# Kernel optimization log

Measured on AMD Instinct MI355X. Metric: run time of the kernel, lower is better.

Reference implementation:

```python
import math
import jax, jax.numpy as jnp
import numpy as np

B, S, M, D, H = 4, 1024, 8, 64, 8
NF = D // 2  # n_freq = head_dim // 2
BANDWIDTH = 1.0


def setup_inputs() -> dict:
    key = jax.random.key(0)
    ks = jax.random.split(key, 12)
    n = lambda k, shp, sc=1.0: (jax.random.normal(k, shp, dtype=jnp.float32) * sc)
    w_scale = 0.02  # typical init scale for linear weights
    return {
        'q_atoms': n(ks[0], (B, S, M, D)),
        'q_logw': n(ks[1], (B, S, M)),
        'k_atoms': n(ks[2], (B, S, M, D)),
        'k_logw': n(ks[3], (B, S, M)),
        'v_atoms': n(ks[4], (B, S, M, D)),
        'v_logw': n(ks[5], (B, S, M)),
        'Wq': n(ks[6], (H * D, D), w_scale),   # torch Linear weight [out, in]
        'Wk': n(ks[7], (H * D, D), w_scale),
        'Wv': n(ks[8], (H * D, D), w_scale),
        'Wo': n(ks[9], (D, H * D), w_scale),
        'Ww': n(ks[10], (M, D), w_scale * 0.1),  # w_proj.weight scaled by 0.1
        'freqs': n(ks[11], (H, D, NF), 1.0 / BANDWIDTH),  # buffer
    }


def reference(q_atoms, q_logw, k_atoms, k_logw, v_atoms, v_logw,
              Wq, Wk, Wv, Wo, Ww, freqs):
    rff_scale = 1.0 / math.sqrt(NF)
    attn_scale = 1.0 / math.sqrt(D)

    q_w = jax.nn.softmax(q_logw, axis=-1)  # [B,S,M]
    k_w = jax.nn.softmax(k_logw, axis=-1)

    def proj(x, W):  # x: [B,S,M,D], W: [H*D, D] -> [B,S,M,H,D]
        return jnp.einsum('bsmd,ed->bsme', x, W).reshape(B, -1, M, H, D)

    qa = proj(q_atoms, Wq)
    ka = proj(k_atoms, Wk)
    va = proj(v_atoms, Wv)  # [B,S,M,H,D]

    def rff_encode(atoms, weights):
        # atoms: [B,S,M,H,D], weights: [B,S,M] -> [B,H,S,F] with F=D
        p = jnp.einsum('bsmhd,hdf->bsmhf', atoms, freqs)
        phi = jnp.concatenate([jnp.cos(p), jnp.sin(p)], axis=-1) * rff_scale
        z = jnp.einsum('bsmhf,bsm->bshf', phi, weights)
        return z.transpose(0, 2, 1, 3)

    q_enc = rff_encode(qa, q_w)  # [B,H,S,D]
    k_enc = rff_encode(ka, k_w)

    attn = jax.nn.softmax(
        jnp.einsum('bhqf,bhkf->bhqk', q_enc, k_enc) * attn_scale, axis=-1)

    # attn @ values, keeping atom dim m: [B,S,M,H,D]
    out = jnp.einsum('bhqk,bkmhd->bqmhd', attn, va)
    out = out.reshape(B, S, M, H * D)
    out_atoms = out @ Wo.T                  # [B,S,M,D]
    out_features = out_atoms.mean(axis=2)   # [B,S,D]
    new_log_weights = q_logw + out_features @ Ww.T  # [B,S,M]
    return out_atoms, new_log_weights
```

## Files before the change

kernel.cpp:

```cpp
#include <hip/hip_runtime.h>
#include <hip/hip_bf16.h>

typedef __hip_bfloat16 bf16;
typedef __attribute__((ext_vector_type(8))) short short8;
typedef __attribute__((ext_vector_type(4))) float floatx4;

#define CB 4
#define CS 1024
#define CM 8
#define CD 64
#define CH 8
#define CNF 32
#define CHD 512

#define OB_STRIDE 520
#define OS_STRIDE 68
#define AT_STRIDE 72
#define VO_STRIDE 40

__device__ __forceinline__ float b2f(bf16 x) { return __bfloat162float(x); }
__device__ __forceinline__ float us2f(unsigned short u) {
    union { unsigned int i; float f; } v; v.i = ((unsigned int)u) << 16; return v.f;
}
__device__ __forceinline__ floatx4 mfma16(short8 a, short8 b, floatx4 c) {
    return __builtin_amdgcn_mfma_f32_16x16x32_bf16(a, b, c, 0, 0, 0);
}


__global__ __launch_bounds__(256) void prep(const float* __restrict__ Wq,
                                            const float* __restrict__ Wk,
                                            const float* __restrict__ freqs,
                                            const float* __restrict__ Wo,
                                            const float* __restrict__ Wv,
                                            bf16* __restrict__ Fqb,
                                            bf16* __restrict__ Fkb,
                                            bf16* __restrict__ Wof,
                                            bf16* __restrict__ Wvf) {
    int bx = blockIdx.x, t = threadIdx.x;
    if (bx < 128) {
        int which = bx >> 6, h = (bx >> 3) & 7, ec = bx & 7;
        const float* W = which ? Wk : Wq;
        bf16* Fb = which ? Fkb : Fqb;
        int f = t & 31, el = t >> 5;
        int e = ec * 8 + el;
        float acc = 0.f;
        for (int d = 0; d < 64; ++d)
            acc += W[(h * 64 + d) * 64 + e] * freqs[(h * 64 + d) * 32 + f];
        int ntile = h * 2 + (f >> 4);
        int half = e >> 5, quad = (e >> 3) & 3, j = e & 7;
        Fb[(ntile * 2 + half) * 512 + quad * 128 + (f & 15) * 8 + j] = __float2bfloat16(acc);
    } else if (bx < 144) {
        int gid = (bx - 128) * 256 + t;
        #pragma unroll
        for (int i = 0; i < 2; ++i) {
            int idx4 = gid * 2 + i;
            float4 v = ((const float4*)Wo)[idx4];
            int flat = idx4 * 4;
            int o = flat >> 9, k0 = flat & 511;
            int ot = o >> 4, r0 = o & 15;
            int ks = k0 >> 5, qd = (k0 >> 3) & 3, j0 = k0 & 7;
            union { bf16 ob[4]; uint2 u; } pk;
            pk.ob[0] = __float2bfloat16(v.x); pk.ob[1] = __float2bfloat16(v.y);
            pk.ob[2] = __float2bfloat16(v.z); pk.ob[3] = __float2bfloat16(v.w);
            *(uint2*)(Wof + (ot * 16 + ks) * 512 + qd * 128 + r0 * 8 + j0) = pk.u;
        }
    } else {
        int gid = (bx - 144) * 256 + t;
        #pragma unroll
        for (int i = 0; i < 2; ++i) {
            int idx4 = gid * 2 + i;
            float4 v = ((const float4*)Wv)[idx4];
            int flat = idx4 * 4;
            int c = flat >> 6, e0 = flat & 63;
            int h2 = c >> 6, d = c & 63;
            int ehalf = e0 >> 5, qd = (e0 >> 3) & 3, j0 = e0 & 7;
            union { bf16 ob[4]; uint2 u; } pk;
            pk.ob[0] = __float2bfloat16(v.x); pk.ob[1] = __float2bfloat16(v.y);
            pk.ob[2] = __float2bfloat16(v.z); pk.ob[3] = __float2bfloat16(v.w);
            *(uint2*)(Wvf + (h2 * 8 + (d >> 4) * 2 + ehalf) * 512
                          + qd * 128 + (d & 15) * 8 + j0) = pk.u;
        }
    }
}

__global__ __launch_bounds__(256) void encvp(const float* __restrict__ qa_in,
                                             const float* __restrict__ ql,
                                             const float* __restrict__ ka_in,
                                             const float* __restrict__ kl,
                                             const bf16* __restrict__ Fqb,
                                             const bf16* __restrict__ Fkb,
                                             bf16* __restrict__ qf,
                                             bf16* __restrict__ kf,
                                             const float* __restrict__ va_in,
                                             const bf16* __restrict__ Wvf,
                                             bf16* __restrict__ Vt) {
    __shared__ __align__(16) bf16 smem[20480];
    int t = threadIdx.x;
    int w = t >> 6, l = t & 63;
    int quad = l >> 4, r = l & 15;

    if (blockIdx.x < 1024) {
        int blk = blockIdx.x;
        int xbase = blk * 4;
        int b = xbase >> 10, s0 = xbase & 1023;
        float* wgtF = (float*)smem;
        bf16* atq = smem + 128;
        bf16* atk = smem + 128 + 2304;
        bf16* zL  = smem + 128 + 4608;
        int tw = w & 1, nb = (w >> 1) * 8;

        {
            const float* srcq = qa_in + (size_t)(blk * 32) * 64;
            const float* srck = ka_in + (size_t)(blk * 32) * 64;
            #pragma unroll
            for (int j = 0; j < 2; ++j) {
                int idx4 = j * 256 + t;
                int flat = idx4 * 4;
                int row = flat >> 6, e = flat & 63;
                float4 vq = ((const float4*)srcq)[idx4];
                float4 vk = ((const float4*)srck)[idx4];
                union { bf16 ob[4]; uint2 u; } pq, pk2;
                pq.ob[0] = __float2bfloat16(vq.x); pq.ob[1] = __float2bfloat16(vq.y);
                pq.ob[2] = __float2bfloat16(vq.z); pq.ob[3] = __float2bfloat16(vq.w);
                pk2.ob[0] = __float2bfloat16(vk.x); pk2.ob[1] = __float2bfloat16(vk.y);
                pk2.ob[2] = __float2bfloat16(vk.z); pk2.ob[3] = __float2bfloat16(vk.w);
                *(uint2*)(atq + row * AT_STRIDE + e) = pq.u;
                *(uint2*)(atk + row * AT_STRIDE + e) = pk2.u;
            }
        }
        if (t < 64) {
            int which = t >> 5, row = t & 31;
            int si = row >> 3, m = row & 7;
            const float* lwp = (which ? kl : ql) + (size_t)(xbase + si) * 8;
            float lw[8]; float mx = -1e30f;
            #pragma unroll
            for (int j = 0; j < 8; ++j) { lw[j] = lwp[j]; mx = fmaxf(mx, lw[j]); }
            float sm = 0.f;
            #pragma unroll
            for (int j = 0; j < 8; ++j) sm += __expf(lw[j] - mx);
            const float rs = 0.17677669529663687f;
            float osc = which ? rs : rs * 0.125f;
            wgtF[which * 32 + row] = __expf(lw[m] - mx) * (osc / sm);
        }
        __syncthreads();

        for (int which = 0; which < 2; ++which) {
            const bf16* atb2 = which ? atk : atq;
            const bf16* Fb = which ? Fkb : Fqb;

            short8 a0 = *(const short8*)(atb2 + (tw * 16 + r) * AT_STRIDE + quad * 8);
            short8 a1 = *(const short8*)(atb2 + (tw * 16 + r) * AT_STRIDE + quad * 8 + 32);

            floatx4 acc[8];
            #pragma unroll
            for (int nt = 0; nt < 8; ++nt) {
                int ntile = nb + nt;
                short8 b0 = *(const short8*)(Fb + (ntile * 2 + 0) * 512 + l * 8);
                short8 b1 = *(const short8*)(Fb + (ntile * 2 + 1) * 512 + l * 8);
                floatx4 c = {0.f, 0.f, 0.f, 0.f};
                c = mfma16(a0, b0, c);
                c = mfma16(a1, b1, c);
                acc[nt] = c;
            }

            float wv[4];
            #pragma unroll
            for (int reg = 0; reg < 4; ++reg)
                wv[reg] = wgtF[which * 32 + tw * 16 + quad * 4 + reg];

            int si = tw * 2 + (quad >> 1);
            int iss = quad & 1;
            #pragma unroll
            for (int nt = 0; nt < 8; ++nt) {
                int n = (nb + nt) * 16 + r;
                int h = n >> 5, f = n & 31;
                float zc = 0.f, zs = 0.f;
                #pragma unroll
                for (int reg = 0; reg < 4; ++reg) {
                    float sv, cv;
                    __sincosf(acc[nt][reg], &sv, &cv);
                    zc += wv[reg] * cv;
                    zs += wv[reg] * sv;
                }
                zc += __shfl_xor(zc, 16);
                zs += __shfl_xor(zs, 16);
                float val = iss ? zs : zc;
                zL[((which * 4 + si) * 8 + h) * 64 + f + 32 * iss] = __float2bfloat16(val);
            }
        }
        __syncthreads();

        #pragma unroll
        for (int rep = 0; rep < 2; ++rep) {
            int idx = rep * 256 + t;
            int row = idx >> 3, c = idx & 7;
            int which = row >> 5, si = (row >> 3) & 3, h = row & 7;
            bf16* enc = which ? kf : qf;
            short8 v = *(const short8*)(zL + row * 64 + c * 8);
            int s = s0 + si;
            int bh = b * 8 + h;
            int kt = s >> 4, half = c >> 2, qd = c & 3;
            *(short8*)(enc + ((size_t)((bh * 64 + kt) * 2 + half)) * 512
                           + (qd * 16 + (s & 15)) * 8) = v;
        }
    } else {
        int vp = blockIdx.x - 1024;
        int bh = vp & 31, sc = vp >> 5;
        int b = bh >> 3, h = bh & 7;
        bf16* atb = smem;
        bf16* os = smem;

        const float* src = va_in + ((size_t)(b * 1024 + sc * 32)) * 512;
        #pragma unroll
        for (int j = 0; j < 16; ++j) {
            int idx4 = j * 256 + t;
            float4 v = ((const float4*)src)[idx4];
            int flat = idx4 * 4;
            int s = flat >> 9, m = (flat >> 6) & 7, e = flat & 63;
            union { bf16 ob[4]; uint2 u; } pk;
            pk.ob[0] = __float2bfloat16(v.x); pk.ob[1] = __float2bfloat16(v.y);
            pk.ob[2] = __float2bfloat16(v.z); pk.ob[3] = __float2bfloat16(v.w);
            *(uint2*)(atb + (m * 32 + s) * AT_STRIDE + e) = pk.u;
        }
        __syncthreads();

        int dhalf = w & 1, sg = w >> 1;
        short8 aw0[2], aw1[2];
        #pragma unroll
        for (int dt = 0; dt < 2; ++dt) {
            int dt4 = dhalf * 2 + dt;
            aw0[dt] = *(const short8*)(Wvf + (size_t)(h * 8 + dt4 * 2 + 0) * 512 + l * 8);
            aw1[dt] = *(const short8*)(Wvf + (size_t)(h * 8 + dt4 * 2 + 1) * 512 + l * 8);
        }
        floatx4 acc[8][2];
        #pragma unroll
        for (int m = 0; m < 8; ++m)
            #pragma unroll
            for (int dt = 0; dt < 2; ++dt) acc[m][dt] = (floatx4){0.f, 0.f, 0.f, 0.f};

        #pragma unroll
        for (int m = 0; m < 8; ++m) {
            short8 b0 = *(const short8*)(atb + (m * 32 + sg * 16 + r) * AT_STRIDE + quad * 8);
            short8 b1 = *(const short8*)(atb + (m * 32 + sg * 16 + r) * AT_STRIDE + quad * 8 + 32);
            #pragma unroll
            for (int dt = 0; dt < 2; ++dt) {
                acc[m][dt] = mfma16(aw0[dt], b0, acc[m][dt]);
                acc[m][dt] = mfma16(aw1[dt], b1, acc[m][dt]);
            }
        }
        __syncthreads();

        #pragma unroll
        for (int m = 0; m < 8; ++m)
            #pragma unroll
            for (int dt = 0; dt < 2; ++dt)
                #pragma unroll
                for (int reg = 0; reg < 4; ++reg) {
                    int n = m * 64 + dhalf * 32 + dt * 16 + quad * 4 + reg;
                    os[n * VO_STRIDE + sg * 16 + r] = __float2bfloat16(acc[m][dt][reg]);
                }
        __syncthreads();

        #pragma unroll
        for (int j = 0; j < 8; ++j) {
            int ch = j * 256 + t;
            int nblk = ch >> 6, lv = ch & 63;
            int rv = lv & 15, qv = lv >> 4;
            short8 v = *(const short8*)(os + (nblk * 16 + rv) * VO_STRIDE + qv * 8);
            *(short8*)(Vt + ((size_t)(bh * 32 + nblk) * 32 + sc) * 512 + lv * 8) = v;
        }
    }
}

__global__ __launch_bounds__(512, 4) void attn_kern(const bf16* __restrict__ qf,
                                                    const bf16* __restrict__ kf,
                                                    const bf16* __restrict__ Vt,
                                                    bf16* __restrict__ tmpf) {
    int n = blockIdx.x;
    int bh = (n & 7) + 8 * (n >> 8);
    int qb = (n >> 3) & 31;
    int b = bh >> 3, h = bh & 7;

    __shared__ __align__(16) bf16 Sc[32 * 1024];
    int t = threadIdx.x;
    int w = t >> 6, l = t & 63;
    int quad = l >> 4, r = l & 15;
    int k7 = r & 7;

    const bf16* qfb = qf + (size_t)(bh * 128 + qb * 4) * 512 + l * 8;
    short8 q0 = *(const short8*)(qfb);
    short8 q1 = *(const short8*)(qfb + 512);
    short8 q2 = *(const short8*)(qfb + 1024);
    short8 q3 = *(const short8*)(qfb + 1536);

    const bf16* kfb = kf + (size_t)(bh * 128) * 512 + l * 8;
    short8 kA0 = *(const short8*)(kfb + (size_t)(w * 8) * 1024);
    short8 kA1 = *(const short8*)(kfb + (size_t)(w * 8) * 1024 + 512);
    short8 kB0 = *(const short8*)(kfb + (size_t)(w * 8 + 1) * 1024);
    short8 kB1 = *(const short8*)(kfb + (size_t)(w * 8 + 1) * 1024 + 512);

    #pragma unroll
    for (int i = 0; i < 8; ++i) {
        short8 k0 = kA0, k1 = kA1;
        kA0 = kB0; kA1 = kB1;
        if (i < 6) {
            kB0 = *(const short8*)(kfb + (size_t)(w * 8 + i + 2) * 1024);
            kB1 = *(const short8*)(kfb + (size_t)(w * 8 + i + 2) * 1024 + 512);
        }
        floatx4 c0 = {0.f, 0.f, 0.f, 0.f}, c1 = {0.f, 0.f, 0.f, 0.f};
        c0 = mfma16(k0, q0, c0); c0 = mfma16(k1, q1, c0);
        c1 = mfma16(k0, q2, c1); c1 = mfma16(k1, q3, c1);
        int ktl = w * 8 + i;
        int chunk = ktl * 2 + (quad >> 1);
        int sw = ((chunk ^ k7) << 3) + (quad & 1) * 4;
        union { uint2 u; bf16 bb[4]; } p0, p1;
        #pragma unroll
        for (int reg = 0; reg < 4; ++reg) {
            p0.bb[reg] = __float2bfloat16(c0[reg]);
            p1.bb[reg] = __float2bfloat16(c1[reg]);
        }
        *(uint2*)(Sc + r * 1024 + sw) = p0.u;
        *(uint2*)(Sc + (r + 16) * 1024 + sw) = p1.u;
    }
    __syncthreads();

    for (int i = 0; i < 4; ++i) {
        int row = w * 4 + i;
        int key = row & 7;
        bf16* rowp = Sc + row * 1024;
        int p0 = ((2 * l) ^ key) << 3;
        int p1 = ((2 * l + 1) ^ key) << 3;
        union { short8 s; unsigned short u[8]; } v0, v1;
        v0.s = *(const short8*)(rowp + p0);
        v1.s = *(const short8*)(rowp + p1);
        float f[16];
        #pragma unroll
        for (int j = 0; j < 8; ++j) { f[j] = us2f(v0.u[j]); f[8 + j] = us2f(v1.u[j]); }
        float mx = -1e30f;
        #pragma unroll
        for (int j = 0; j < 16; ++j) mx = fmaxf(mx, f[j]);
        #pragma unroll
        for (int off = 32; off; off >>= 1) mx = fmaxf(mx, __shfl_xor(mx, off));
        float sm = 0.f;
        #pragma unroll
        for (int j = 0; j < 16; ++j) { f[j] = __expf(f[j] - mx); sm += f[j]; }
        #pragma unroll
        for (int off = 32; off; off >>= 1) sm += __shfl_xor(sm, off);
        float inv = 1.f / sm;
        #pragma unroll
        for (int j = 0; j < 8; ++j) {
            v0.u[j] = (unsigned short)(__bfloat16_as_ushort(__float2bfloat16(f[j] * inv)));
            v1.u[j] = (unsigned short)(__bfloat16_as_ushort(__float2bfloat16(f[8 + j] * inv)));
        }
        *(short8*)(rowp + p0) = v0.s;
        *(short8*)(rowp + p1) = v1.s;
    }
    __syncthreads();

    floatx4 acc0[4], acc1[4];
    #pragma unroll
    for (int nt = 0; nt < 4; ++nt) {
        acc0[nt] = (floatx4){0.f, 0.f, 0.f, 0.f};
        acc1[nt] = (floatx4){0.f, 0.f, 0.f, 0.f};
    }
    const bf16* vbase = Vt + ((size_t)(bh * 32 + w * 4) * 32) * 512 + l * 8;
    short8 vA[4], vB[4], vC[4];
    #pragma unroll
    for (int nt = 0; nt < 4; ++nt) vA[nt] = *(const short8*)(vbase + nt * 16384);
    #pragma unroll
    for (int nt = 0; nt < 4; ++nt) vB[nt] = *(const short8*)(vbase + nt * 16384 + 512);

    #pragma unroll
    for (int ks = 0; ks < 32; ++ks) {
        if (ks < 30) {
            #pragma unroll
            for (int nt = 0; nt < 4; ++nt)
                vC[nt] = *(const short8*)(vbase + nt * 16384 + (ks + 2) * 512);
        }
        int pc = (((ks * 4 + quad) ^ k7) << 3);
        short8 pa0 = *(const short8*)(Sc + r * 1024 + pc);
        short8 pa1 = *(const short8*)(Sc + (16 + r) * 1024 + pc);
        #pragma unroll
        for (int nt = 0; nt < 4; ++nt) {
            acc0[nt] = mfma16(pa0, vA[nt], acc0[nt]);
            acc1[nt] = mfma16(pa1, vA[nt], acc1[nt]);
        }
        #pragma unroll
        for (int nt = 0; nt < 4; ++nt) { vA[nt] = vB[nt]; vB[nt] = vC[nt]; }
    }
    __syncthreads();

    bf16* Ob = Sc;
    #pragma unroll
    for (int nt = 0; nt < 4; ++nt)
        #pragma unroll
        for (int reg = 0; reg < 4; ++reg) {
            int col = w * 64 + nt * 16 + r;
            int m = col >> 6, d = col & 63;
            int colS = m * 64 + ((d + m * 8) & 63);
            Ob[(quad * 4 + reg) * OB_STRIDE + colS] = __float2bfloat16(acc0[nt][reg]);
            Ob[(quad * 4 + reg + 16) * OB_STRIDE + colS] = __float2bfloat16(acc1[nt][reg]);
        }
    __syncthreads();

    #pragma unroll
    for (int i = 0; i < 4; ++i) {
        int ci = i * 8 + w;
        int lv = t & 63;
        int T = ci >> 1, khalf = ci & 1;
        int quadv = lv >> 4, rv = lv & 15;
        int p = rv >> 3, m = rv & 7;
        int q_local = T * 2 + p;
        int d0 = khalf * 32 + quadv * 8;
        int colS = m * 64 + ((d0 + m * 8) & 63);
        short8 v = *(const short8*)(Ob + q_local * OB_STRIDE + colS);
        int GT = b * 512 + qb * 16 + T;
        *(short8*)(tmpf + ((size_t)(GT * 16 + h * 2 + khalf)) * 512 + lv * 8) = v;
    }
}

__global__ __launch_bounds__(256) void finalize(const bf16* __restrict__ tmpf,
                                                const bf16* __restrict__ Wof,
                                                const float* __restrict__ Ww,
                                                const float* __restrict__ ql,
                                                float* __restrict__ out) {
    __shared__ __align__(16) float Os[64][OS_STRIDE];
    __shared__ float fs[8][64];
    int t = threadIdx.x;
    int w = t >> 6, l = t & 63;
    int quad = l >> 4, r = l & 15;
    size_t rowbase = (size_t)blockIdx.x * 64;

    floatx4 acc[4];
    #pragma unroll
    for (int nt = 0; nt < 4; ++nt) acc[nt] = (floatx4){0.f, 0.f, 0.f, 0.f};

    const bf16* afrag = tmpf + ((size_t)(blockIdx.x * 4 + w) * 16) * 512 + l * 8;
    const bf16* bfrag = Wof + l * 8;

    for (int ks = 0; ks < 16; ++ks) {
        short8 a = *(const short8*)(afrag + ks * 512);
        #pragma unroll
        for (int nt = 0; nt < 4; ++nt) {
            short8 bb = *(const short8*)(bfrag + (size_t)(nt * 16 + ks) * 512);
            acc[nt] = mfma16(a, bb, acc[nt]);
        }
    }
    #pragma unroll
    for (int nt = 0; nt < 4; ++nt)
        #pragma unroll
        for (int reg = 0; reg < 4; ++reg)
            Os[w * 16 + quad * 4 + reg][nt * 16 + r] = acc[nt][reg];
    __syncthreads();

    #pragma unroll
    for (int i = 0; i < 4; ++i) {
        int ch = i * 256 + t;
        int rr = ch >> 4, c4 = (ch & 15) * 4;
        float4 v = *(const float4*)&Os[rr][c4];
        *(float4*)(out + (rowbase + rr) * 64 + c4) = v;
    }

    {
        int g = t >> 5, oo = (t & 31) * 2;
        float f0 = 0.f, f1 = 0.f;
        #pragma unroll
        for (int m = 0; m < 8; ++m) {
            f0 += Os[g * 8 + m][oo];
            f1 += Os[g * 8 + m][oo + 1];
        }
        fs[g][oo] = f0 * 0.125f;
        fs[g][oo + 1] = f1 * 0.125f;
    }
    __syncthreads();

    if (t < 64) {
        int g = t >> 3, mm = t & 7;
        size_t x = (size_t)blockIdx.x * 8 + g;
        float nl = ql[x * 8 + mm];
        #pragma unroll
        for (int o = 0; o < 64; ++o) nl += fs[g][o] * Ww[mm * 64 + o];
        out[(size_t)CB * CS * CM * CD + x * 8 + mm] = nl;
    }
}

extern "C" void kernel_launch(void* const* d_in, const int* in_sizes, int n_in,
                              void* d_out, int out_size, void* d_ws, size_t ws_size,
                              hipStream_t stream) {
    const float* q_atoms = (const float*)d_in[0];
    const float* q_logw  = (const float*)d_in[1];
    const float* k_atoms = (const float*)d_in[2];
    const float* k_logw  = (const float*)d_in[3];
    const float* v_atoms = (const float*)d_in[4];
    const float* Wq = (const float*)d_in[6];
    const float* Wk = (const float*)d_in[7];
    const float* Wv = (const float*)d_in[8];
    const float* Wo = (const float*)d_in[9];
    const float* Ww = (const float*)d_in[10];
    const float* freqs = (const float*)d_in[11];

    bf16* Fqb = (bf16*)d_ws;
    bf16* Fkb = Fqb + 16384;
    bf16* qf = Fkb + 16384;
    bf16* kf = qf + 2097152;
    bf16* Vt = kf + 2097152;
    bf16* tmpf = Vt + 2097152 * 8;
    bf16* Wof = tmpf + 16777216;
    bf16* Wvf = Wof + 32768;
    float* out = (float*)d_out;

    prep<<<160, 256, 0, stream>>>(Wq, Wk, freqs, Wo, Wv, Fqb, Fkb, Wof, Wvf);
    encvp<<<2048, 256, 0, stream>>>(q_atoms, q_logw, k_atoms, k_logw,
                                    Fqb, Fkb, qf, kf,
                                    v_atoms, Wvf, Vt);
    attn_kern<<<1024, 512, 0, stream>>>(qf, kf, Vt, tmpf);
    finalize<<<CB * CS / 8, 256, 0, stream>>>(tmpf, Wof, Ww, q_logw, out);
}
```

Before: 185.9 us.

## Double query tile per attention block to reuse K and V loads

Each attention block now handles 64 query rows instead of 32, so every K and V fragment it loads feeds four MFMA query tiles instead of two. The grid is halved and shared memory for scores doubles to 128KB. This cuts global K/V traffic per query and raises MFMA work per load. In exchange it uses more registers and lowers occupancy, which is declared as 2 blocks per CU. With only 512 blocks, fewer waves are available to hide latency.

```diff
diff --git a/kernel.cpp b/kernel.cpp
--- a/kernel.cpp
+++ b/kernel.cpp
@@ -272,26 +272,25 @@
     }
 }
 
-__global__ __launch_bounds__(512, 4) void attn_kern(const bf16* __restrict__ qf,
+__global__ __launch_bounds__(512, 2) void attn_kern(const bf16* __restrict__ qf,
                                                     const bf16* __restrict__ kf,
                                                     const bf16* __restrict__ Vt,
                                                     bf16* __restrict__ tmpf) {
     int n = blockIdx.x;
-    int bh = (n & 7) + 8 * (n >> 8);
-    int qb = (n >> 3) & 31;
+    int bh = (n & 7) | (((n >> 7) & 3) << 3);
+    int qb = (n >> 3) & 15;
     int b = bh >> 3, h = bh & 7;
 
-    __shared__ __align__(16) bf16 Sc[32 * 1024];
+    __shared__ __align__(16) bf16 Sc[64 * 1024];
     int t = threadIdx.x;
     int w = t >> 6, l = t & 63;
     int quad = l >> 4, r = l & 15;
     int k7 = r & 7;
 
-    const bf16* qfb = qf + (size_t)(bh * 128 + qb * 4) * 512 + l * 8;
-    short8 q0 = *(const short8*)(qfb);
-    short8 q1 = *(const short8*)(qfb + 512);
-    short8 q2 = *(const short8*)(qfb + 1024);
-    short8 q3 = *(const short8*)(qfb + 1536);
+    const bf16* qfb = qf + (size_t)(bh * 128 + qb * 8) * 512 + l * 8;
+    short8 q[8];
+    #pragma unroll
+    for (int i = 0; i < 8; ++i) q[i] = *(const short8*)(qfb + i * 512);
 
     const bf16* kfb = kf + (size_t)(bh * 128) * 512 + l * 8;
     short8 kA0 = *(const short8*)(kfb + (size_t)(w * 8) * 1024);
@@ -307,25 +306,24 @@
             kB0 = *(const short8*)(kfb + (size_t)(w * 8 + i + 2) * 1024);
             kB1 = *(const short8*)(kfb + (size_t)(w * 8 + i + 2) * 1024 + 512);
         }
-        floatx4 c0 = {0.f, 0.f, 0.f, 0.f}, c1 = {0.f, 0.f, 0.f, 0.f};
-        c0 = mfma16(k0, q0, c0); c0 = mfma16(k1, q1, c0);
-        c1 = mfma16(k0, q2, c1); c1 = mfma16(k1, q3, c1);
         int ktl = w * 8 + i;
         int chunk = ktl * 2 + (quad >> 1);
         int sw = ((chunk ^ k7) << 3) + (quad & 1) * 4;
-        union { uint2 u; bf16 bb[4]; } p0, p1;
-        #pragma unroll
-        for (int reg = 0; reg < 4; ++reg) {
-            p0.bb[reg] = __float2bfloat16(c0[reg]);
-            p1.bb[reg] = __float2bfloat16(c1[reg]);
-        }
-        *(uint2*)(Sc + r * 1024 + sw) = p0.u;
-        *(uint2*)(Sc + (r + 16) * 1024 + sw) = p1.u;
+        #pragma unroll
+        for (int qt = 0; qt < 4; ++qt) {
+            floatx4 c = {0.f, 0.f, 0.f, 0.f};
+            c = mfma16(k0, q[2 * qt], c);
+            c = mfma16(k1, q[2 * qt + 1], c);
+            union { uint2 u; bf16 bb[4]; } p;
+            #pragma unroll
+            for (int reg = 0; reg < 4; ++reg) p.bb[reg] = __float2bfloat16(c[reg]);
+            *(uint2*)(Sc + (qt * 16 + r) * 1024 + sw) = p.u;
+        }
     }
     __syncthreads();
 
-    for (int i = 0; i < 4; ++i) {
-        int row = w * 4 + i;
+    for (int i = 0; i < 8; ++i) {
+        int row = w * 8 + i;
         int key = row & 7;
         bf16* rowp = Sc + row * 1024;
         int p0 = ((2 * l) ^ key) << 3;
@@ -357,12 +355,12 @@
     }
     __syncthreads();
 
-    floatx4 acc0[4], acc1[4];
-    #pragma unroll
-    for (int nt = 0; nt < 4; ++nt) {
-        acc0[nt] = (floatx4){0.f, 0.f, 0.f, 0.f};
-        acc1[nt] = (floatx4){0.f, 0.f, 0.f, 0.f};
-    }
+    floatx4 acc[4][4];
+    #pragma unroll
+    for (int qt = 0; qt < 4; ++qt)
+        #pragma unroll
+        for (int nt = 0; nt < 4; ++nt) acc[qt][nt] = (floatx4){0.f, 0.f, 0.f, 0.f};
+
     const bf16* vbase = Vt + ((size_t)(bh * 32 + w * 4) * 32) * 512 + l * 8;
     short8 vA[4], vB[4], vC[4];
     #pragma unroll
@@ -378,13 +376,15 @@
                 vC[nt] = *(const short8*)(vbase + nt * 16384 + (ks + 2) * 512);
         }
         int pc = (((ks * 4 + quad) ^ k7) << 3);
-        short8 pa0 = *(const short8*)(Sc + r * 1024 + pc);
-        short8 pa1 = *(const short8*)(Sc + (16 + r) * 1024 + pc);
-        #pragma unroll
-        for (int nt = 0; nt < 4; ++nt) {
-            acc0[nt] = mfma16(pa0, vA[nt], acc0[nt]);
-            acc1[nt] = mfma16(pa1, vA[nt], acc1[nt]);
-        }
+        short8 pa[4];
+        #pragma unroll
+        for (int qt = 0; qt < 4; ++qt)
+            pa[qt] = *(const short8*)(Sc + (qt * 16 + r) * 1024 + pc);
+        #pragma unroll
+        for (int nt = 0; nt < 4; ++nt)
+            #pragma unroll
+            for (int qt = 0; qt < 4; ++qt)
+                acc[qt][nt] = mfma16(pa[qt], vA[nt], acc[qt][nt]);
         #pragma unroll
         for (int nt = 0; nt < 4; ++nt) { vA[nt] = vB[nt]; vB[nt] = vC[nt]; }
     }
@@ -392,19 +392,21 @@
 
     bf16* Ob = Sc;
     #pragma unroll
-    for (int nt = 0; nt < 4; ++nt)
-        #pragma unroll
-        for (int reg = 0; reg < 4; ++reg) {
-            int col = w * 64 + nt * 16 + r;
-            int m = col >> 6, d = col & 63;
-            int colS = m * 64 + ((d + m * 8) & 63);
-            Ob[(quad * 4 + reg) * OB_STRIDE + colS] = __float2bfloat16(acc0[nt][reg]);
-            Ob[(quad * 4 + reg + 16) * OB_STRIDE + colS] = __float2bfloat16(acc1[nt][reg]);
-        }
+    for (int qt = 0; qt < 4; ++qt)
+        #pragma unroll
+        for (int nt = 0; nt < 4; ++nt)
+            #pragma unroll
+            for (int reg = 0; reg < 4; ++reg) {
+                int col = w * 64 + nt * 16 + r;
+                int m = col >> 6, d = col & 63;
+                int colS = m * 64 + ((d + m * 8) & 63);
+                Ob[(qt * 16 + quad * 4 + reg) * OB_STRIDE + colS] =
+                    __float2bfloat16(acc[qt][nt][reg]);
+            }
     __syncthreads();
 
     #pragma unroll
-    for (int i = 0; i < 4; ++i) {
+    for (int i = 0; i < 8; ++i) {
         int ci = i * 8 + w;
         int lv = t & 63;
         int T = ci >> 1, khalf = ci & 1;
@@ -414,7 +416,7 @@
         int d0 = khalf * 32 + quadv * 8;
         int colS = m * 64 + ((d0 + m * 8) & 63);
         short8 v = *(const short8*)(Ob + q_local * OB_STRIDE + colS);
-        int GT = b * 512 + qb * 16 + T;
+        int GT = b * 512 + qb * 32 + T;
         *(short8*)(tmpf + ((size_t)(GT * 16 + h * 2 + khalf)) * 512 + lv * 8) = v;
     }
 }
@@ -513,6 +515,6 @@
     encvp<<<2048, 256, 0, stream>>>(q_atoms, q_logw, k_atoms, k_logw,
                                     Fqb, Fkb, qf, kf,
                                     v_atoms, Wvf, Vt);
-    attn_kern<<<1024, 512, 0, stream>>>(qf, kf, Vt, tmpf);
+    attn_kern<<<512, 512, 0, stream>>>(qf, kf, Vt, tmpf);
     finalize<<<CB * CS / 8, 256, 0, stream>>>(tmpf, Wof, Ww, q_logw, out);
 }
```

Result: slower. 190.6 us (+2.6%).

## Deepen K/V register prefetch, raise MFMA priority, drop softmax max pass

Applied to the files above, without the earlier changes.

The K-tile and V-tile loads in the attention kernel now use a 4-deep rotating register buffer instead of a 2-deep one, so global-load latency is hidden further ahead. The P·V MFMA block is wrapped in s_setprio to favour matrix issue over other waves. The row-max reduction in the softmax is removed, which relies on the RFF dot products being bounded (|score| stays small) so exp cannot overflow. V-projection blocks are reordered h-major so neighbouring blocks share head weights. The cost is higher VGPR pressure from the larger buffers, which may lower occupancy.

```diff
diff --git a/kernel.cpp b/kernel.cpp
--- a/kernel.cpp
+++ b/kernel.cpp
@@ -205,8 +205,9 @@
         }
     } else {
         int vp = blockIdx.x - 1024;
-        int bh = vp & 31, sc = vp >> 5;
-        int b = bh >> 3, h = bh & 7;
+        int g = vp & 127, h = vp >> 7;
+        int b = g >> 5, sc = g & 31;
+        int bh = b * 8 + h;
         bf16* atb = smem;
         bf16* os = smem;
 
@@ -294,18 +295,19 @@
     short8 q3 = *(const short8*)(qfb + 1536);
 
     const bf16* kfb = kf + (size_t)(bh * 128) * 512 + l * 8;
-    short8 kA0 = *(const short8*)(kfb + (size_t)(w * 8) * 1024);
-    short8 kA1 = *(const short8*)(kfb + (size_t)(w * 8) * 1024 + 512);
-    short8 kB0 = *(const short8*)(kfb + (size_t)(w * 8 + 1) * 1024);
-    short8 kB1 = *(const short8*)(kfb + (size_t)(w * 8 + 1) * 1024 + 512);
+    short8 kr[4][2];
+    #pragma unroll
+    for (int d = 0; d < 4; ++d) {
+        kr[d][0] = *(const short8*)(kfb + (size_t)(w * 8 + d) * 1024);
+        kr[d][1] = *(const short8*)(kfb + (size_t)(w * 8 + d) * 1024 + 512);
+    }
 
     #pragma unroll
     for (int i = 0; i < 8; ++i) {
-        short8 k0 = kA0, k1 = kA1;
-        kA0 = kB0; kA1 = kB1;
-        if (i < 6) {
-            kB0 = *(const short8*)(kfb + (size_t)(w * 8 + i + 2) * 1024);
-            kB1 = *(const short8*)(kfb + (size_t)(w * 8 + i + 2) * 1024 + 512);
+        short8 k0 = kr[i & 3][0], k1 = kr[i & 3][1];
+        if (i + 4 < 8) {
+            kr[i & 3][0] = *(const short8*)(kfb + (size_t)(w * 8 + i + 4) * 1024);
+            kr[i & 3][1] = *(const short8*)(kfb + (size_t)(w * 8 + i + 4) * 1024 + 512);
         }
         floatx4 c0 = {0.f, 0.f, 0.f, 0.f}, c1 = {0.f, 0.f, 0.f, 0.f};
         c0 = mfma16(k0, q0, c0); c0 = mfma16(k1, q1, c0);
@@ -336,14 +338,9 @@
         float f[16];
         #pragma unroll
         for (int j = 0; j < 8; ++j) { f[j] = us2f(v0.u[j]); f[8 + j] = us2f(v1.u[j]); }
-        float mx = -1e30f;
-        #pragma unroll
-        for (int j = 0; j < 16; ++j) mx = fmaxf(mx, f[j]);
-        #pragma unroll
-        for (int off = 32; off; off >>= 1) mx = fmaxf(mx, __shfl_xor(mx, off));
         float sm = 0.f;
         #pragma unroll
-        for (int j = 0; j < 16; ++j) { f[j] = __expf(f[j] - mx); sm += f[j]; }
+        for (int j = 0; j < 16; ++j) { f[j] = __expf(f[j]); sm += f[j]; }
         #pragma unroll
         for (int off = 32; off; off >>= 1) sm += __shfl_xor(sm, off);
         float inv = 1.f / sm;
@@ -364,29 +361,30 @@
         acc1[nt] = (floatx4){0.f, 0.f, 0.f, 0.f};
     }
     const bf16* vbase = Vt + ((size_t)(bh * 32 + w * 4) * 32) * 512 + l * 8;
-    short8 vA[4], vB[4], vC[4];
-    #pragma unroll
-    for (int nt = 0; nt < 4; ++nt) vA[nt] = *(const short8*)(vbase + nt * 16384);
-    #pragma unroll
-    for (int nt = 0; nt < 4; ++nt) vB[nt] = *(const short8*)(vbase + nt * 16384 + 512);
+    short8 vr[4][4];
+    #pragma unroll
+    for (int d = 0; d < 4; ++d)
+        #pragma unroll
+        for (int nt = 0; nt < 4; ++nt)
+            vr[d][nt] = *(const short8*)(vbase + nt * 16384 + d * 512);
 
     #pragma unroll
     for (int ks = 0; ks < 32; ++ks) {
-        if (ks < 30) {
-            #pragma unroll
-            for (int nt = 0; nt < 4; ++nt)
-                vC[nt] = *(const short8*)(vbase + nt * 16384 + (ks + 2) * 512);
-        }
         int pc = (((ks * 4 + quad) ^ k7) << 3);
         short8 pa0 = *(const short8*)(Sc + r * 1024 + pc);
         short8 pa1 = *(const short8*)(Sc + (16 + r) * 1024 + pc);
+        __builtin_amdgcn_s_setprio(1);
         #pragma unroll
         for (int nt = 0; nt < 4; ++nt) {
-            acc0[nt] = mfma16(pa0, vA[nt], acc0[nt]);
-            acc1[nt] = mfma16(pa1, vA[nt], acc1[nt]);
-        }
-        #pragma unroll
-        for (int nt = 0; nt < 4; ++nt) { vA[nt] = vB[nt]; vB[nt] = vC[nt]; }
+            acc0[nt] = mfma16(pa0, vr[ks & 3][nt], acc0[nt]);
+            acc1[nt] = mfma16(pa1, vr[ks & 3][nt], acc1[nt]);
+        }
+        __builtin_amdgcn_s_setprio(0);
+        if (ks + 4 < 32) {
+            #pragma unroll
+            for (int nt = 0; nt < 4; ++nt)
+                vr[ks & 3][nt] = *(const short8*)(vbase + nt * 16384 + (ks + 4) * 512);
+        }
     }
     __syncthreads();
 
```

After: 173.0 us. 1.07x faster.
